# Kernel optimization log

Hardware: AMD Instinct MI355X
Metric: run time of the kernel (lower is better)

Reference implementation:

```python
import jax, jax.numpy as jnp
import numpy as np

N = 50000
E = 800000
C = 96

def _lin_params(key, fan_in, fan_out):
    k1, k2 = jax.random.split(key)
    bound = 1.0 / np.sqrt(fan_in)
    W = jax.random.uniform(k1, (fan_in, fan_out), minval=-bound, maxval=bound, dtype=jnp.float32)
    b = jax.random.uniform(k2, (fan_out,), minval=-bound, maxval=bound, dtype=jnp.float32)
    return W, b

def setup_inputs() -> dict:
    key = jax.random.key(0)
    ks = jax.random.split(key, 10)
    x = jax.random.normal(ks[0], (N, C), dtype=jnp.float32)
    edge_index = jax.random.randint(ks[1], (2, E), 0, N, dtype=jnp.int64)
    edge_attr = jax.random.normal(ks[2], (E, 1), dtype=jnp.float32)
    W_l0, b_l0 = _lin_params(ks[3], 1, C)   # linear0: 1 -> C
    W_l1, b_l1 = _lin_params(ks[4], C, C)   # linear1: C -> C
    W00, b00 = _lin_params(ks[5], C, C)     # gine0 mlp layer 0
    W01, b01 = _lin_params(ks[6], C, C)     # gine0 mlp layer 1
    W10, b10 = _lin_params(ks[7], C, C)     # gine1 mlp layer 0
    W11, b11 = _lin_params(ks[8], C, C)     # gine1 mlp layer 1
    return {"x": x, "edge_index": edge_index, "edge_attr": edge_attr,
            "W_l0": W_l0, "b_l0": b_l0, "W_l1": W_l1, "b_l1": b_l1,
            "W00": W00, "b00": b00, "W01": W01, "b01": b01,
            "W10": W10, "b10": b10, "W11": W11, "b11": b11}

def _gine_conv(x, src, dst, e, W1, b1, W2, b2):
    # message: relu(x_j + e) gathered from source nodes, scatter-added to targets
    msg = jax.nn.relu(x[src] + e)                     # [E, C]
    agg = jax.ops.segment_sum(msg, dst, num_segments=x.shape[0])  # [N, C]
    h = x + agg                                       # eps = 0 (PyG default)
    h = jax.nn.relu(h @ W1 + b1)
    h = jax.nn.relu(h @ W2 + b2)
    return h

def reference(x, edge_index, edge_attr, W_l0, b_l0, W_l1, b_l1,
              W00, b00, W01, b01, W10, b10, W11, b11):
    src, dst = edge_index[0], edge_index[1]
    e = jax.nn.relu(edge_attr @ W_l0 + b_l0) @ W_l1 + b_l1  # [E, C]
    h = _gine_conv(x, src, dst, e, W00, b00, W01, b01)
    h = jax.nn.relu(h)
    h = _gine_conv(h, src, dst, e, W10, b10, W11, b11)
    h = jax.nn.relu(h)
    return h
```

## Files before the change

kernel.cpp:

```cpp
#include <hip/hip_runtime.h>
#include <hip/hip_fp16.h>
#include <math.h>

#define Nn 50000
#define Ee 800000
#define Cc 96

#define NPB 196
#define NBK 256
#define P2_T 512
#define P2_E 4
#define P2_BLK (P2_T * P2_E)
#define NB2 ((Ee + P2_BLK - 1) / P2_BLK)

typedef __attribute__((ext_vector_type(8))) __bf16 bf16x8;
typedef __attribute__((ext_vector_type(4))) float f32x4;

__device__ inline void split_bf16(float v, unsigned short& hi, unsigned short& lo) {
    unsigned u = __float_as_uint(v);
    hi = (unsigned short)(u >> 16);
    float rem = v - __uint_as_float(((unsigned)hi) << 16);
    lo = (unsigned short)(__float_as_uint(rem) >> 16);
}

__device__ inline bool edge_valid(int s, int d) {
    return (unsigned)s < (unsigned)Nn && (unsigned)d < (unsigned)Nn;
}

__global__ __launch_bounds__(128) void build_table_kernel(
        const float* __restrict__ Wl0, const float* __restrict__ bl0,
        const float* __restrict__ Wl1, const float* __restrict__ bl1,
        float* __restrict__ st, float* __restrict__ tabf) {
    __shared__ float rt[Cc], rw[Cc], rb[Cc];
    __shared__ float sst[Cc], ssw[Cc], ssb[Cc];
    __shared__ int sso[Cc];
    int c = threadIdx.x;
    if (c < Cc) {
        float w = Wl0[c], b = bl0[c];
        rt[c] = (w != 0.0f) ? (-b / w) : INFINITY;
        rw[c] = w; rb[c] = b;
    }
    __syncthreads();
    if (c < Cc) {
        float t = rt[c];
        int r = 0;
        for (int jj = 0; jj < Cc; ++jj) {
            float tj = rt[jj];
            r += (tj < t || (tj == t && jj < c)) ? 1 : 0;
        }
        sst[r] = t; ssw[r] = rw[c]; ssb[r] = rb[c]; sso[r] = c;
    }
    __syncthreads();
    if (blockIdx.x == 0 && c < Cc) st[c] = sst[c];
    int k = blockIdx.x;
    if (c < Cc) {
        float a = 0.f, bacc = bl1[c];
        for (int i = 0; i < Cc; ++i) {
            float w = ssw[i], b = ssb[i];
            float wv = Wl1[sso[i] * Cc + c];
            bool act = (w > 0.f) ? (i < k) : ((w < 0.f) ? (i >= k) : (b > 0.f));
            if (act) { a = fmaf(w, wv, a); bacc = fmaf(b, wv, bacc); }
        }
        int base = k * (2 * Cc) + (c >> 1) * 4 + ((c & 1) << 1);
        tabf[base] = a;
        tabf[base + 1] = bacc;
    }
}

__global__ __launch_bounds__(96) void wsplit_kernel(
        const float* __restrict__ W0, const float* __restrict__ W1,
        const float* __restrict__ W2, const float* __restrict__ W3,
        unsigned short* __restrict__ wsp) {
    int mat = blockIdx.x / 96, n = blockIdx.x % 96, k = threadIdx.x;
    const float* W = (mat == 0) ? W0 : (mat == 1) ? W1 : (mat == 2) ? W2 : W3;
    float v = W[k * 96 + n];
    unsigned short hi, lo;
    split_bf16(v, hi, lo);
    unsigned short* base = wsp + (size_t)mat * 2 * 9216;
    base[n * 96 + k] = hi;
    base[9216 + n * 96 + k] = lo;
}

__global__ __launch_bounds__(256) void cvt16_kernel(const float* __restrict__ in,
                                                    __half* __restrict__ out) {
    const int n4 = Nn * Cc / 4;
    for (int i = blockIdx.x * blockDim.x + threadIdx.x; i < n4; i += gridDim.x * blockDim.x) {
        float4 v = ((const float4*)in)[i];
        ((__half2*)out)[2 * i] = __floats2half2_rn(v.x, v.y);
        ((__half2*)out)[2 * i + 1] = __floats2half2_rn(v.z, v.w);
    }
}

__global__ __launch_bounds__(P2_T) void bucket_hist_kernel(const int* __restrict__ ei,
                                                           int* __restrict__ bmat) {
    __shared__ int cnt[NBK];
    int tid = threadIdx.x;
    for (int i = tid; i < NBK; i += P2_T) cnt[i] = 0;
    __syncthreads();
    int base = blockIdx.x * P2_BLK;
    for (int t = 0; t < P2_E; ++t) {
        int e = base + tid + t * P2_T;
        if (e < Ee) {
            int s = ei[e], d = ei[Ee + e];
            if (edge_valid(s, d)) atomicAdd(&cnt[d / NPB], 1);
        }
    }
    __syncthreads();
    for (int i = tid; i < NBK; i += P2_T) bmat[blockIdx.x * NBK + i] = cnt[i];
}

__global__ __launch_bounds__(512) void bmat_scan_kernel(const int* __restrict__ bmat,
                                                        int* __restrict__ boffrel,
                                                        int* __restrict__ btot) {
    __shared__ int lds[512];
    int bk = blockIdx.x, t = threadIdx.x;
    int v = (t < NB2) ? bmat[t * NBK + bk] : 0;
    lds[t] = v;
    __syncthreads();
    for (int o = 1; o < 512; o <<= 1) {
        int u = (t >= o) ? lds[t - o] : 0;
        __syncthreads();
        lds[t] += u;
        __syncthreads();
    }
    if (t < NB2) boffrel[t * NBK + bk] = lds[t] - v;
    if (t == 511) btot[bk] = lds[511];
}

__global__ __launch_bounds__(256) void btot_scan_kernel(const int* __restrict__ btot,
                                                        int* __restrict__ bbase) {
    __shared__ int lds[256];
    int t = threadIdx.x;
    int v = btot[t];
    lds[t] = v;
    __syncthreads();
    for (int o = 1; o < 256; o <<= 1) {
        int u = (t >= o) ? lds[t - o] : 0;
        __syncthreads();
        lds[t] += u;
        __syncthreads();
    }
    bbase[t] = lds[t] - v;
}

__global__ __launch_bounds__(P2_T) void pass2_kernel(const int* __restrict__ ei,
                                                     const float* __restrict__ eattr,
                                                     const int* __restrict__ boffrel,
                                                     const int* __restrict__ bbase,
                                                     int2* __restrict__ stage) {
    __shared__ int curs[NBK];
    int tid = threadIdx.x;
    for (int i = tid; i < NBK; i += P2_T)
        curs[i] = bbase[i] + boffrel[blockIdx.x * NBK + i];
    __syncthreads();
    int base = blockIdx.x * P2_BLK;
    for (int t = 0; t < P2_E; ++t) {
        int e = base + tid + t * P2_T;
        if (e >= Ee) continue;
        int s = ei[e], d = ei[Ee + e];
        if (!edge_valid(s, d)) continue;
        int bk = d / NPB, dl = d - bk * NPB;
        int pos = atomicAdd(&curs[bk], 1);
        stage[pos] = make_int2(s | (dl << 16), __float_as_int(eattr[e]));
    }
}

__global__ __launch_bounds__(512) void pass3_kernel(const int2* __restrict__ stage,
                                                    const int* __restrict__ bbase,
                                                    const int* __restrict__ btot,
                                                    const float* __restrict__ st,
                                                    int* __restrict__ rowptr,
                                                    int2* __restrict__ me) {
    __shared__ int cnt[NPB];
    __shared__ int scn[256];
    __shared__ int curs[NPB];
    __shared__ float ts[Cc];
    int bk = blockIdx.x, tid = threadIdx.x;
    if (tid < Cc) ts[tid] = st[tid];
    for (int i = tid; i < NPB; i += 512) cnt[i] = 0;
    __syncthreads();
    int seg0 = bbase[bk], segn = btot[bk];
    for (int p = tid; p < segn; p += 512)
        atomicAdd(&cnt[(stage[seg0 + p].x >> 16) & 0xFF], 1);
    __syncthreads();
    if (tid < 256) scn[tid] = (tid < NPB) ? cnt[tid] : 0;
    __syncthreads();
    for (int o = 1; o < 256; o <<= 1) {
        int u = (tid < 256 && tid >= o) ? scn[tid - o] : 0;
        __syncthreads();
        if (tid < 256) scn[tid] += u;
        __syncthreads();
    }
    int nstart = bk * NPB;
    if (tid < NPB) {
        int node = nstart + tid;
        if (node < Nn) {
            int e0 = seg0 + scn[tid] - cnt[tid];
            rowptr[node] = e0;
            curs[tid] = e0;
        }
    }
    if (bk == NBK - 1 && tid == 0) rowptr[Nn] = seg0 + segn;
    __syncthreads();
    for (int p = tid; p < segn; p += 512) {
        int2 sv = stage[seg0 + p];
        unsigned sx = (unsigned)sv.x;
        int src = sx & 0xFFFF;
        int dl = (sx >> 16) & 0xFF;
        float ea = __int_as_float(sv.y);
        int lo = 0, hi = Cc;
        while (lo < hi) { int m = (lo + hi) >> 1; if (ts[m] < ea) lo = m + 1; else hi = m; }
        int pos = atomicAdd(&curs[dl], 1);
        me[pos] = make_int2((int)((unsigned)(src * 192) | ((unsigned)lo << 24)), sv.y);
    }
}

#define AGG_NB 512
__global__ __launch_bounds__(1024) void aggregate_kernel(
        const float* __restrict__ feat, const __half* __restrict__ feat16,
        const int* __restrict__ rowptr, const int2* __restrict__ me,
        const float4* __restrict__ tab, float* __restrict__ out) {
    __shared__ float4 tl[(Cc + 1) * 48];
    int tid = threadIdx.x;
    for (int i = tid; i < (Cc + 1) * 48; i += 1024) tl[i] = tab[i];
    __syncthreads();
    int wave = tid >> 6, lane = tid & 63;
    if (lane >= 48) return;
    int j = lane;
    const float2* f2 = (const float2*)feat;
    const char* gb = (const char*)feat16;
    int j4 = j << 2;
    for (int node = blockIdx.x * 16 + wave; node < Nn; node += AGG_NB * 16) {
        float2 acc = f2[(size_t)node * 48 + j];
        int s = rowptr[node], e = rowptr[node + 1];
        int p = s;
        for (; p + 4 <= e; p += 4) {
            int2 m0 = me[p], m1 = me[p + 1], m2 = me[p + 2], m3 = me[p + 3];
            unsigned x0 = (unsigned)m0.x, x1 = (unsigned)m1.x;
            unsigned x2 = (unsigned)m2.x, x3 = (unsigned)m3.x;
            __half2 h0 = *(const __half2*)(gb + (x0 & 0xFFFFFF) + j4);
            __half2 h1 = *(const __half2*)(gb + (x1 & 0xFFFFFF) + j4);
            __half2 h2 = *(const __half2*)(gb + (x2 & 0xFFFFFF) + j4);
            __half2 h3 = *(const __half2*)(gb + (x3 & 0xFFFFFF) + j4);
            float4 t0 = tl[(x0 >> 24) * 48 + j];
            float4 t1 = tl[(x1 >> 24) * 48 + j];
            float4 t2 = tl[(x2 >> 24) * 48 + j];
            float4 t3 = tl[(x3 >> 24) * 48 + j];
            float2 f0 = __half22float2(h0), f1 = __half22float2(h1);
            float2 fb2 = __half22float2(h2), f3 = __half22float2(h3);
            float ea0 = __int_as_float(m0.y), ea1 = __int_as_float(m1.y);
            float ea2 = __int_as_float(m2.y), ea3 = __int_as_float(m3.y);
            acc.x += fmaxf(f0.x + fmaf(ea0, t0.x, t0.y), 0.f);
            acc.y += fmaxf(f0.y + fmaf(ea0, t0.z, t0.w), 0.f);
            acc.x += fmaxf(f1.x + fmaf(ea1, t1.x, t1.y), 0.f);
            acc.y += fmaxf(f1.y + fmaf(ea1, t1.z, t1.w), 0.f);
            acc.x += fmaxf(fb2.x + fmaf(ea2, t2.x, t2.y), 0.f);
            acc.y += fmaxf(fb2.y + fmaf(ea2, t2.z, t2.w), 0.f);
            acc.x += fmaxf(f3.x + fmaf(ea3, t3.x, t3.y), 0.f);
            acc.y += fmaxf(f3.y + fmaf(ea3, t3.z, t3.w), 0.f);
        }
        for (; p < e; ++p) {
            int2 m0 = me[p];
            unsigned x0 = (unsigned)m0.x;
            float2 f0 = __half22float2(*(const __half2*)(gb + (x0 & 0xFFFFFF) + j4));
            float4 t0 = tl[(x0 >> 24) * 48 + j];
            float ea0 = __int_as_float(m0.y);
            acc.x += fmaxf(f0.x + fmaf(ea0, t0.x, t0.y), 0.f);
            acc.y += fmaxf(f0.y + fmaf(ea0, t0.z, t0.w), 0.f);
        }
        ((float2*)out)[(size_t)node * 48 + j] = acc;
    }
}

#define MLP_PAD 104
__global__ __launch_bounds__(256) void mlp2_kernel(
        const float* __restrict__ in,
        const unsigned short* __restrict__ wh1, const unsigned short* __restrict__ wl1,
        const float* __restrict__ b1g,
        const unsigned short* __restrict__ wh2, const unsigned short* __restrict__ wl2,
        const float* __restrict__ b2g, float* __restrict__ out,
        __half* __restrict__ out16) {
    __shared__ __attribute__((aligned(16))) unsigned short xh[64 * MLP_PAD], xl[64 * MLP_PAD];
    __shared__ __attribute__((aligned(16))) unsigned short wth[96 * MLP_PAD], wtl[96 * MLP_PAD];
    __shared__ float bb1[Cc], bb2[Cc];
    int tid = threadIdx.x;
    int row0 = blockIdx.x * 64;

    for (int t = 0; t < 24; ++t) {
        int idx = tid + t * 256;
        int r = idx / Cc, c = idx - r * Cc;
        int gr = row0 + r;
        float v = (gr < Nn) ? in[(size_t)gr * Cc + c] : 0.f;
        unsigned short hi, lo;
        split_bf16(v, hi, lo);
        xh[r * MLP_PAD + c] = hi; xl[r * MLP_PAD + c] = lo;
    }
    for (int i = tid; i < 1152; i += 256) {
        int n = i / 12, kc = (i % 12) * 8;
        *(uint4*)&wth[n * MLP_PAD + kc] = *(const uint4*)&wh1[n * 96 + kc];
        *(uint4*)&wtl[n * MLP_PAD + kc] = *(const uint4*)&wl1[n * 96 + kc];
    }
    if (tid < Cc) { bb1[tid] = b1g[tid]; bb2[tid] = b2g[tid]; }
    __syncthreads();

    int lane = tid & 63, w = tid >> 6;
    int li = lane & 15, lg = lane >> 4;
    int arow = w * 16 + li;

    f32x4 acc[6];
    for (int nt = 0; nt < 6; ++nt) {
        float bv = bb1[nt * 16 + li];
        acc[nt] = (f32x4){bv, bv, bv, bv};
    }
    for (int k0 = 0; k0 < Cc; k0 += 32) {
        int ko = k0 + lg * 8;
        bf16x8 ah = *(const bf16x8*)&xh[arow * MLP_PAD + ko];
        bf16x8 al = *(const bf16x8*)&xl[arow * MLP_PAD + ko];
        for (int nt = 0; nt < 6; ++nt) {
            bf16x8 bh = *(const bf16x8*)&wth[(nt * 16 + li) * MLP_PAD + ko];
            bf16x8 bl = *(const bf16x8*)&wtl[(nt * 16 + li) * MLP_PAD + ko];
            acc[nt] = __builtin_amdgcn_mfma_f32_16x16x32_bf16(ah, bh, acc[nt], 0, 0, 0);
            acc[nt] = __builtin_amdgcn_mfma_f32_16x16x32_bf16(ah, bl, acc[nt], 0, 0, 0);
            acc[nt] = __builtin_amdgcn_mfma_f32_16x16x32_bf16(al, bh, acc[nt], 0, 0, 0);
        }
    }
    __syncthreads();
    for (int nt = 0; nt < 6; ++nt) {
        for (int r = 0; r < 4; ++r) {
            float v = fmaxf(acc[nt][r], 0.f);
            int row = w * 16 + lg * 4 + r;
            int col = nt * 16 + li;
            unsigned short hi, lo;
            split_bf16(v, hi, lo);
            xh[row * MLP_PAD + col] = hi; xl[row * MLP_PAD + col] = lo;
        }
    }
    for (int i = tid; i < 1152; i += 256) {
        int n = i / 12, kc = (i % 12) * 8;
        *(uint4*)&wth[n * MLP_PAD + kc] = *(const uint4*)&wh2[n * 96 + kc];
        *(uint4*)&wtl[n * MLP_PAD + kc] = *(const uint4*)&wl2[n * 96 + kc];
    }
    __syncthreads();

    for (int nt = 0; nt < 6; ++nt) {
        float bv = bb2[nt * 16 + li];
        acc[nt] = (f32x4){bv, bv, bv, bv};
    }
    for (int k0 = 0; k0 < Cc; k0 += 32) {
        int ko = k0 + lg * 8;
        bf16x8 ah = *(const bf16x8*)&xh[arow * MLP_PAD + ko];
        bf16x8 al = *(const bf16x8*)&xl[arow * MLP_PAD + ko];
        for (int nt = 0; nt < 6; ++nt) {
            bf16x8 bh = *(const bf16x8*)&wth[(nt * 16 + li) * MLP_PAD + ko];
            bf16x8 bl = *(const bf16x8*)&wtl[(nt * 16 + li) * MLP_PAD + ko];
            acc[nt] = __builtin_amdgcn_mfma_f32_16x16x32_bf16(ah, bh, acc[nt], 0, 0, 0);
            acc[nt] = __builtin_amdgcn_mfma_f32_16x16x32_bf16(ah, bl, acc[nt], 0, 0, 0);
            acc[nt] = __builtin_amdgcn_mfma_f32_16x16x32_bf16(al, bh, acc[nt], 0, 0, 0);
        }
    }
    for (int nt = 0; nt < 6; ++nt) {
        for (int r = 0; r < 4; ++r) {
            int grow = row0 + w * 16 + lg * 4 + r;
            if (grow < Nn) {
                float v = fmaxf(acc[nt][r], 0.f);
                out[(size_t)grow * Cc + nt * 16 + li] = v;
                if (out16) out16[(size_t)grow * Cc + nt * 16 + li] = __float2half_rn(v);
            }
        }
    }
}

extern "C" void kernel_launch(void* const* d_in, const int* in_sizes, int n_in,
                              void* d_out, int out_size, void* d_ws, size_t ws_size,
                              hipStream_t stream) {
    const float* x     = (const float*)d_in[0];
    const int*   ei    = (const int*)d_in[1];
    const float* eattr = (const float*)d_in[2];
    const float* Wl0   = (const float*)d_in[3];
    const float* bl0   = (const float*)d_in[4];
    const float* Wl1   = (const float*)d_in[5];
    const float* bl1   = (const float*)d_in[6];
    const float* W00   = (const float*)d_in[7];
    const float* b00   = (const float*)d_in[8];
    const float* W01   = (const float*)d_in[9];
    const float* b01   = (const float*)d_in[10];
    const float* W10   = (const float*)d_in[11];
    const float* b10   = (const float*)d_in[12];
    const float* W11   = (const float*)d_in[13];
    const float* b11   = (const float*)d_in[14];
    float* outp = (float*)d_out;

    char* w = (char*)d_ws;
    size_t off = 0;
    auto alloc = [&](size_t bytes) { size_t r = off; off += (bytes + 255) & ~(size_t)255; return r; };
    int*   rowptr  = (int*)  (w + alloc((size_t)(Nn + 1) * 4));
    int2*  me      = (int2*) (w + alloc((size_t)Ee * 8));
    float* st      = (float*)(w + alloc((size_t)Cc * 4));
    int*   bmat    = (int*)  (w + alloc((size_t)NB2 * NBK * 4));
    int*   boffrel = (int*)  (w + alloc((size_t)NB2 * NBK * 4));
    int*   btot    = (int*)  (w + alloc((size_t)NBK * 4));
    int*   bbase   = (int*)  (w + alloc((size_t)NBK * 4));
    float* tabf    = (float*)(w + alloc((size_t)(Cc + 1) * 2 * Cc * 4));
    unsigned short* wsp = (unsigned short*)(w + alloc((size_t)4 * 2 * 9216 * 2));
    float* hpre    = (float*)(w + alloc((size_t)Nn * Cc * 4));
    __half* g16    = (__half*)(w + alloc((size_t)Nn * Cc * 2));
    int2*  stage   = (int2*)hpre;
    (void)ws_size; (void)in_sizes; (void)n_in; (void)out_size;

    build_table_kernel<<<Cc + 1, 128, 0, stream>>>(Wl0, bl0, Wl1, bl1, st, tabf);
    wsplit_kernel<<<384, 96, 0, stream>>>(W00, W01, W10, W11, wsp);
    bucket_hist_kernel<<<NB2, P2_T, 0, stream>>>(ei, bmat);
    bmat_scan_kernel<<<NBK, 512, 0, stream>>>(bmat, boffrel, btot);
    btot_scan_kernel<<<1, 256, 0, stream>>>(btot, bbase);
    pass2_kernel<<<NB2, P2_T, 0, stream>>>(ei, eattr, boffrel, bbase, stage);
    pass3_kernel<<<NBK, 512, 0, stream>>>(stage, bbase, btot, st, rowptr, me);
    cvt16_kernel<<<1024, 256, 0, stream>>>(x, g16);

    const float4* tab = (const float4*)tabf;
    const unsigned short* wh00 = wsp;
    const unsigned short* wl00 = wsp + 9216;
    const unsigned short* wh01 = wsp + 18432;
    const unsigned short* wl01 = wsp + 27648;
    const unsigned short* wh10 = wsp + 36864;
    const unsigned short* wl10 = wsp + 46080;
    const unsigned short* wh11 = wsp + 55296;
    const unsigned short* wl11 = wsp + 64512;

    aggregate_kernel<<<AGG_NB, 1024, 0, stream>>>(x, g16, rowptr, me, tab, hpre);
    mlp2_kernel<<<(Nn + 63) / 64, 256, 0, stream>>>(hpre, wh00, wl00, b00, wh01, wl01, b01, hpre, g16);
    aggregate_kernel<<<AGG_NB, 1024, 0, stream>>>(hpre, g16, rowptr, me, tab, outp);
    mlp2_kernel<<<(Nn + 63) / 64, 256, 0, stream>>>(outp, wh10, wl10, b10, wh11, wl11, b11, outp, (__half*)nullptr);
}
```

Measured before the change: 196.8 us.

## Split fp16 feature gather into per-XCD channel slices for L2 locality

Stores the fp16 node features as four channel slices of 24 channels each, each slice 2.4MB. Aggregate blocks are mapped by block index modulo 8 so that each pair of XCDs gathers from only one slice. This shrinks each XCD's gather working set so it fits better in its private L2. In exchange each wave now handles four nodes with 12 active lanes each, so every node's edge list is read four times (once per slice), and the half-precision writes from the MLP and the conversion kernel become scattered.

After: 212.1 us. 7.8% more time.

```diff
diff --git a/kernel.cpp b/kernel.cpp
--- a/kernel.cpp
+++ b/kernel.cpp
@@ -5,6 +5,9 @@
 #define Nn 50000
 #define Ee 800000
 #define Cc 96
+
+#define NSL 4
+#define SLICE_BYTES ((size_t)Nn * 48)
 
 #define NPB 196
 #define NBK 256
@@ -82,12 +85,14 @@
 }
 
 __global__ __launch_bounds__(256) void cvt16_kernel(const float* __restrict__ in,
-                                                    __half* __restrict__ out) {
-    const int n4 = Nn * Cc / 4;
-    for (int i = blockIdx.x * blockDim.x + threadIdx.x; i < n4; i += gridDim.x * blockDim.x) {
-        float4 v = ((const float4*)in)[i];
-        ((__half2*)out)[2 * i] = __floats2half2_rn(v.x, v.y);
-        ((__half2*)out)[2 * i + 1] = __floats2half2_rn(v.z, v.w);
+                                                    __half* __restrict__ g16s) {
+    const int np = Nn * 48;
+    for (int i = blockIdx.x * blockDim.x + threadIdx.x; i < np; i += gridDim.x * blockDim.x) {
+        int node = i / 48, jg = i - node * 48;
+        float2 v = ((const float2*)in)[i];
+        int z = jg / 12, jp = jg - z * 12;
+        *(__half2*)((char*)g16s + (size_t)z * SLICE_BYTES + (size_t)node * 48 + jp * 4) =
+            __floats2half2_rn(v.x, v.y);
     }
 }
 
@@ -211,41 +216,50 @@
         int lo = 0, hi = Cc;
         while (lo < hi) { int m = (lo + hi) >> 1; if (ts[m] < ea) lo = m + 1; else hi = m; }
         int pos = atomicAdd(&curs[dl], 1);
-        me[pos] = make_int2((int)((unsigned)(src * 192) | ((unsigned)lo << 24)), sv.y);
+        me[pos] = make_int2((int)((unsigned)(src * 48) | ((unsigned)lo << 24)), sv.y);
     }
 }
 
 #define AGG_NB 512
+#define AGG_STRIDE ((AGG_NB / NSL) * 64)
 __global__ __launch_bounds__(1024) void aggregate_kernel(
-        const float* __restrict__ feat, const __half* __restrict__ feat16,
+        const float* __restrict__ feat, const __half* __restrict__ g16s,
         const int* __restrict__ rowptr, const int2* __restrict__ me,
         const float4* __restrict__ tab, float* __restrict__ out) {
-    __shared__ float4 tl[(Cc + 1) * 48];
+    __shared__ float4 tl[(Cc + 1) * 12];
+    int b = blockIdx.x;
+    int xcd = b & 7;
+    int z = xcd >> 1;
+    int wb = ((b >> 3) << 1) + (xcd & 1);
     int tid = threadIdx.x;
-    for (int i = tid; i < (Cc + 1) * 48; i += 1024) tl[i] = tab[i];
+    for (int i = tid; i < (Cc + 1) * 12; i += 1024) {
+        int k = i / 12, jp = i - k * 12;
+        tl[i] = tab[k * 48 + z * 12 + jp];
+    }
     __syncthreads();
     int wave = tid >> 6, lane = tid & 63;
-    if (lane >= 48) return;
-    int j = lane;
-    const float2* f2 = (const float2*)feat;
-    const char* gb = (const char*)feat16;
-    int j4 = j << 2;
-    for (int node = blockIdx.x * 16 + wave; node < Nn; node += AGG_NB * 16) {
-        float2 acc = f2[(size_t)node * 48 + j];
+    int g = lane >> 4, il = lane & 15;
+    if (il >= 12) return;
+    const char* gb = (const char*)g16s + (size_t)z * SLICE_BYTES;
+    int il4 = il << 2;
+    int cbase = z * 24 + (il << 1);
+    int slot = wave * 4 + g;
+    for (int node = wb * 64 + slot; node < Nn; node += AGG_STRIDE) {
+        float2 acc = *(const float2*)&feat[(size_t)node * Cc + cbase];
         int s = rowptr[node], e = rowptr[node + 1];
         int p = s;
         for (; p + 4 <= e; p += 4) {
             int2 m0 = me[p], m1 = me[p + 1], m2 = me[p + 2], m3 = me[p + 3];
             unsigned x0 = (unsigned)m0.x, x1 = (unsigned)m1.x;
             unsigned x2 = (unsigned)m2.x, x3 = (unsigned)m3.x;
-            __half2 h0 = *(const __half2*)(gb + (x0 & 0xFFFFFF) + j4);
-            __half2 h1 = *(const __half2*)(gb + (x1 & 0xFFFFFF) + j4);
-            __half2 h2 = *(const __half2*)(gb + (x2 & 0xFFFFFF) + j4);
-            __half2 h3 = *(const __half2*)(gb + (x3 & 0xFFFFFF) + j4);
-            float4 t0 = tl[(x0 >> 24) * 48 + j];
-            float4 t1 = tl[(x1 >> 24) * 48 + j];
-            float4 t2 = tl[(x2 >> 24) * 48 + j];
-            float4 t3 = tl[(x3 >> 24) * 48 + j];
+            __half2 h0 = *(const __half2*)(gb + (x0 & 0xFFFFFF) + il4);
+            __half2 h1 = *(const __half2*)(gb + (x1 & 0xFFFFFF) + il4);
+            __half2 h2 = *(const __half2*)(gb + (x2 & 0xFFFFFF) + il4);
+            __half2 h3 = *(const __half2*)(gb + (x3 & 0xFFFFFF) + il4);
+            float4 t0 = tl[(x0 >> 24) * 12 + il];
+            float4 t1 = tl[(x1 >> 24) * 12 + il];
+            float4 t2 = tl[(x2 >> 24) * 12 + il];
+            float4 t3 = tl[(x3 >> 24) * 12 + il];
             float2 f0 = __half22float2(h0), f1 = __half22float2(h1);
             float2 fb2 = __half22float2(h2), f3 = __half22float2(h3);
             float ea0 = __int_as_float(m0.y), ea1 = __int_as_float(m1.y);
@@ -262,13 +276,13 @@
         for (; p < e; ++p) {
             int2 m0 = me[p];
             unsigned x0 = (unsigned)m0.x;
-            float2 f0 = __half22float2(*(const __half2*)(gb + (x0 & 0xFFFFFF) + j4));
-            float4 t0 = tl[(x0 >> 24) * 48 + j];
+            float2 f0 = __half22float2(*(const __half2*)(gb + (x0 & 0xFFFFFF) + il4));
+            float4 t0 = tl[(x0 >> 24) * 12 + il];
             float ea0 = __int_as_float(m0.y);
             acc.x += fmaxf(f0.x + fmaf(ea0, t0.x, t0.y), 0.f);
             acc.y += fmaxf(f0.y + fmaf(ea0, t0.z, t0.w), 0.f);
         }
-        ((float2*)out)[(size_t)node * 48 + j] = acc;
+        *(float2*)&out[(size_t)node * Cc + cbase] = acc;
     }
 }
 
@@ -363,8 +377,15 @@
             int grow = row0 + w * 16 + lg * 4 + r;
             if (grow < Nn) {
                 float v = fmaxf(acc[nt][r], 0.f);
-                out[(size_t)grow * Cc + nt * 16 + li] = v;
-                if (out16) out16[(size_t)grow * Cc + nt * 16 + li] = __float2half_rn(v);
+                int col = nt * 16 + li;
+                out[(size_t)grow * Cc + col] = v;
+                if (out16) {
+                    int jg = col >> 1;
+                    int z = jg / 12, jp = jg - z * 12;
+                    *(__half*)((char*)out16 + (size_t)z * SLICE_BYTES +
+                               (size_t)grow * 48 + jp * 4 + ((col & 1) << 1)) =
+                        __float2half_rn(v);
+                }
             }
         }
     }
@@ -403,7 +424,7 @@
     float* tabf    = (float*)(w + alloc((size_t)(Cc + 1) * 2 * Cc * 4));
     unsigned short* wsp = (unsigned short*)(w + alloc((size_t)4 * 2 * 9216 * 2));
     float* hpre    = (float*)(w + alloc((size_t)Nn * Cc * 4));
-    __half* g16    = (__half*)(w + alloc((size_t)Nn * Cc * 2));
+    __half* g16    = (__half*)(w + alloc(NSL * SLICE_BYTES));
     int2*  stage   = (int2*)hpre;
     (void)ws_size; (void)in_sizes; (void)n_in; (void)out_size;
 
```
